# Kernel tuning notes

Hardware: AMD Instinct MI355X
Metric: run time of the kernel (lower is better)

The kernel has to match this reference:

```python
import jax, jax.numpy as jnp
import numpy as np

B, T, C = 2, 1024, 1024
E, F, K = 8, 2048, 2


def setup_inputs() -> dict:
    key = jax.random.key(0)
    ks = jax.random.split(key, 5)
    s = 1.0 / np.sqrt(C)
    return {
        "x": jax.random.normal(ks[0], (B, T, C), jnp.float32),
        "Wr": jax.random.normal(ks[1], (E, C), jnp.float32) * s,   # router weight [E, d_model]
        "w1": jax.random.normal(ks[2], (E, C, F), jnp.float32) * s, # gate proj per expert
        "w3": jax.random.normal(ks[3], (E, C, F), jnp.float32) * s, # up proj per expert
        "w2": jax.random.normal(ks[4], (E, F, C), jnp.float32) * (1.0 / np.sqrt(F)),  # down proj
    }


def reference(x, Wr, w1, w3, w2):
    Bq, Tq, Cq = x.shape
    flat = x.reshape(-1, Cq)                          # [N, C]
    N = flat.shape[0]
    probs = jax.nn.softmax(flat @ Wr.T, axis=-1)      # [N, E]
    topw, topi = jax.lax.top_k(probs, K)              # [N, K]
    topw = topw / jnp.sum(topw, axis=-1, keepdims=True)
    # dense gate matrix: zero for unselected experts (same math as masked loop)
    gates = jnp.zeros((N, E), flat.dtype).at[jnp.arange(N)[:, None], topi].set(topw)
    # evaluate all experts, weight by gates (gate=0 kills unrouted experts)
    h1 = jnp.einsum('nd,edf->nef', flat, w1)          # [N, E, F]
    h3 = jnp.einsum('nd,edf->nef', flat, w3)
    h = jax.nn.silu(h1) * h3
    y = jnp.einsum('nef,efd->ned', h, w2)             # [N, E, C]
    out = jnp.einsum('ned,ne->nd', y, gates)          # [N, C]
    return out.reshape(Bq, Tq, Cq)
```

## Files before the change

### kernel.cpp

```cpp
#include <hip/hip_runtime.h>
#include <math.h>

typedef _Float16 f16;
typedef _Float16 f16x2 __attribute__((ext_vector_type(2)));
typedef _Float16 f16x4 __attribute__((ext_vector_type(4)));
typedef _Float16 f16x8 __attribute__((ext_vector_type(8)));
typedef __fp16 h16x2 __attribute__((ext_vector_type(2)));
typedef float f32x4 __attribute__((ext_vector_type(4)));

#define N_TOK 2048
#define C_DIM 1024
#define E_NUM 8
#define F_DIM 2048
#define MAXTILES 40

#define WS_COUNTS    0
#define WS_OFFSETS   64
#define WS_TILESTART 128
#define WS_CURSOR    192
#define WS_TOPI      256
#define WS_TOPW      (WS_TOPI + 16384)
#define WS_ROWS      (WS_TOPW + 16384)
#define WS_SLOT      (WS_ROWS + 16384)
#define WS_X16       (1u << 20)
#define WS_H         (6u << 20)
#define WS_Y0        (23u << 20)
#define WS_Y1        (32u << 20)

__device__ __forceinline__ void glds16(const void* g, void* l) {
  __builtin_amdgcn_global_load_lds((const __attribute__((address_space(1))) void*)g,
                                   (__attribute__((address_space(3))) void*)l, 16, 0, 0);
}

__device__ __forceinline__ f16x2 pkrtz(float a, float b) {
  union { h16x2 h; f16x2 f; } u;
  u.h = __builtin_amdgcn_cvt_pkrtz(a, b);
  return u.f;
}

__global__ void cvtx_kernel(const float* __restrict__ x, f16* __restrict__ x16) {
  int i = (blockIdx.x * 256 + threadIdx.x) * 8;
  f32x4 a = *(const f32x4*)(x + i);
  f32x4 b = *(const f32x4*)(x + i + 4);
  union { f16x8 v; f16x2 h[4]; } u;
  u.h[0] = pkrtz(a[0], a[1]);
  u.h[1] = pkrtz(a[2], a[3]);
  u.h[2] = pkrtz(b[0], b[1]);
  u.h[3] = pkrtz(b[2], b[3]);
  *(f16x8*)(x16 + i) = u.v;
}

__global__ void router_kernel(const float* __restrict__ x, const float* __restrict__ Wr,
                              int* counts, int* topi, float* topw) {
  int tok = blockIdx.x * 4 + (threadIdx.x >> 6);
  int lane = threadIdx.x & 63;
  const float* xr = x + (size_t)tok * C_DIM;
  float xv[16];
#pragma unroll
  for (int i = 0; i < 16; ++i) xv[i] = xr[i * 64 + lane];
  float logit[E_NUM];
#pragma unroll
  for (int e = 0; e < E_NUM; ++e) {
    const float* wr = Wr + (size_t)e * C_DIM;
    float acc = 0.f;
#pragma unroll
    for (int i = 0; i < 16; ++i) acc += xv[i] * wr[i * 64 + lane];
#pragma unroll
    for (int s = 1; s < 64; s <<= 1) acc += __shfl_xor(acc, s, 64);
    logit[e] = acc;
  }
  if (lane == 0) {
    float m = logit[0];
#pragma unroll
    for (int e = 1; e < E_NUM; ++e) m = fmaxf(m, logit[e]);
    float p[E_NUM];
#pragma unroll
    for (int e = 0; e < E_NUM; ++e) p[e] = expf(logit[e] - m);
    float p0 = -1.f, p1 = -1.f;
    int i0 = 0, i1 = 0;
#pragma unroll
    for (int e = 0; e < E_NUM; ++e) {
      float v = p[e];
      if (v > p0) { p1 = p0; i1 = i0; p0 = v; i0 = e; }
      else if (v > p1) { p1 = v; i1 = e; }
    }
    float inv = 1.f / (p0 + p1);
    topi[2 * tok] = i0; topi[2 * tok + 1] = i1;
    topw[2 * tok] = p0 * inv; topw[2 * tok + 1] = p1 * inv;
    atomicAdd(&counts[i0], 1);
    atomicAdd(&counts[i1], 1);
  }
}

__global__ void scan_kernel(const int* counts, int* offsets, int* tilestart, int* cursor) {
  if (threadIdx.x == 0) {
    int o = 0, t = 0;
    for (int e = 0; e < E_NUM; ++e) {
      offsets[e] = o; tilestart[e] = t; cursor[e] = o;
      o += counts[e];
      t += (counts[e] + 127) >> 7;
    }
    offsets[E_NUM] = o; tilestart[E_NUM] = t;
  }
}

__global__ void scatter_kernel(const int* __restrict__ topi, int* cursor,
                               int* rows_perm, int* slot_of) {
  int n = blockIdx.x * blockDim.x + threadIdx.x;
  if (n >= N_TOK) return;
#pragma unroll
  for (int k = 0; k < 2; ++k) {
    int e = topi[2 * n + k];
    int pos = atomicAdd(&cursor[e], 1);
    rows_perm[pos] = n;
    slot_of[2 * n + k] = pos;
  }
}

__launch_bounds__(256, 2)
__global__ void upproj_kernel(const f16* __restrict__ x16,
                              const float* __restrict__ w1,
                              const float* __restrict__ w3,
                              const int* __restrict__ counts,
                              const int* __restrict__ offsets,
                              const int* __restrict__ tilestart,
                              const int* __restrict__ rows_perm,
                              f16* __restrict__ h_buf) {
  __shared__ f16 A_lds[128 * 32];
  __shared__ f16 B1_lds[128 * 32];
  __shared__ f16 B3_lds[128 * 32];

  int rt = blockIdx.y;
  int e = -1;
#pragma unroll
  for (int i = 0; i < E_NUM; ++i)
    if (rt >= tilestart[i] && rt < tilestart[i + 1]) e = i;
  if (e < 0) return;
  int row0 = (rt - tilestart[e]) * 128;
  int cnt = counts[e];
  int off = offsets[e];
  int f0 = blockIdx.x * 128;
  int t = threadIdx.x, wid = t >> 6, lane = t & 63;

  const f16* asrc[2];
#pragma unroll
  for (int p = 0; p < 2; ++p) {
    int chunk = p * 256 + t, row = chunk >> 2, cc = chunk & 3;
    int lr = row0 + row; if (lr > cnt - 1) lr = cnt - 1;
    int g = rows_perm[off + lr];
    asrc[p] = x16 + (size_t)g * C_DIM + 8 * (cc ^ ((row >> 1) & 3));
  }
  f16* adst0 = A_lds + wid * 512;
  f16* adst1 = A_lds + (4 + wid) * 512;

  int bcol = t & 127;
  int bg = t >> 7;
  int bxor = (bcol >> 1) & 3;
  const size_t eb = (size_t)e * C_DIM * F_DIM;
  const float* w1p = w1 + eb + (size_t)(bg * 16) * F_DIM + f0 + bcol;
  const float* w3p = w3 + eb + (size_t)(bg * 16) * F_DIM + f0 + bcol;

  f32x4 acc1[4][4] = {};
  f32x4 acc3[4][4] = {};
  int wr = (wid >> 1) * 64, wc = (wid & 1) * 64;
  int fr = lane & 15, fq = lane >> 4;

  for (int k0 = 0; k0 < C_DIM; k0 += 32) {
    __syncthreads();
    glds16(asrc[0] + k0, adst0);
    glds16(asrc[1] + k0, adst1);
    {
      float v[16];
#pragma unroll
      for (int j = 0; j < 16; ++j) v[j] = w1p[(size_t)(k0 + j) * F_DIM];
#pragma unroll
      for (int q = 0; q < 4; ++q) {
        union { f16x4 v4; f16x2 h2[2]; } u;
        u.h2[0] = pkrtz(v[q * 4 + 0], v[q * 4 + 1]);
        u.h2[1] = pkrtz(v[q * 4 + 2], v[q * 4 + 3]);
        int k = bg * 16 + q * 4;
        *(f16x4*)&B1_lds[bcol * 32 + ((k >> 3) ^ bxor) * 8 + (k & 7)] = u.v4;
      }
#pragma unroll
      for (int j = 0; j < 16; ++j) v[j] = w3p[(size_t)(k0 + j) * F_DIM];
#pragma unroll
      for (int q = 0; q < 4; ++q) {
        union { f16x4 v4; f16x2 h2[2]; } u;
        u.h2[0] = pkrtz(v[q * 4 + 0], v[q * 4 + 1]);
        u.h2[1] = pkrtz(v[q * 4 + 2], v[q * 4 + 3]);
        int k = bg * 16 + q * 4;
        *(f16x4*)&B3_lds[bcol * 32 + ((k >> 3) ^ bxor) * 8 + (k & 7)] = u.v4;
      }
    }
    __syncthreads();

    f16x8 a[4];
#pragma unroll
    for (int m = 0; m < 4; ++m) {
      int row = wr + m * 16 + fr;
      a[m] = *(const f16x8*)&A_lds[row * 32 + (fq ^ ((row >> 1) & 3)) * 8];
    }
    f16x8 b[4];
#pragma unroll
    for (int n = 0; n < 4; ++n) {
      int col = wc + n * 16 + fr;
      b[n] = *(const f16x8*)&B1_lds[col * 32 + (fq ^ ((col >> 1) & 3)) * 8];
    }
#pragma unroll
    for (int m = 0; m < 4; ++m)
#pragma unroll
      for (int n = 0; n < 4; ++n)
        acc1[m][n] = __builtin_amdgcn_mfma_f32_16x16x32_f16(a[m], b[n], acc1[m][n], 0, 0, 0);
#pragma unroll
    for (int n = 0; n < 4; ++n) {
      int col = wc + n * 16 + fr;
      b[n] = *(const f16x8*)&B3_lds[col * 32 + (fq ^ ((col >> 1) & 3)) * 8];
    }
#pragma unroll
    for (int m = 0; m < 4; ++m)
#pragma unroll
      for (int n = 0; n < 4; ++n)
        acc3[m][n] = __builtin_amdgcn_mfma_f32_16x16x32_f16(a[m], b[n], acc3[m][n], 0, 0, 0);
  }

#pragma unroll
  for (int m = 0; m < 4; ++m)
#pragma unroll
    for (int n = 0; n < 4; ++n)
#pragma unroll
      for (int i = 0; i < 4; ++i) {
        int lr = row0 + wr + m * 16 + fq * 4 + i;
        if (lr < cnt) {
          float v1 = acc1[m][n][i], v3 = acc3[m][n][i];
          float hval = v1 / (1.f + expf(-v1)) * v3;
          h_buf[(size_t)(off + lr) * F_DIM + f0 + wc + n * 16 + fr] = (f16)hval;
        }
      }
}

__launch_bounds__(256, 2)
__global__ void downproj_kernel(const f16* __restrict__ h_buf,
                                const float* __restrict__ w2,
                                const int* __restrict__ counts,
                                const int* __restrict__ offsets,
                                const int* __restrict__ tilestart,
                                f16* __restrict__ y0,
                                f16* __restrict__ y1) {
  __shared__ f16 A_lds[128 * 32];
  __shared__ f16 B_lds[128 * 32];

  int kh = blockIdx.z;
  f16* yb = kh ? y1 : y0;
  int rt = blockIdx.y;
  int e = -1;
#pragma unroll
  for (int i = 0; i < E_NUM; ++i)
    if (rt >= tilestart[i] && rt < tilestart[i + 1]) e = i;
  if (e < 0) return;
  int row0 = (rt - tilestart[e]) * 128;
  int cnt = counts[e];
  int off = offsets[e];
  int c0 = blockIdx.x * 128;
  int t = threadIdx.x, wid = t >> 6, lane = t & 63;

  const f16* asrc[2];
#pragma unroll
  for (int p = 0; p < 2; ++p) {
    int chunk = p * 256 + t, row = chunk >> 2, cc = chunk & 3;
    int lr = row0 + row; if (lr > cnt - 1) lr = cnt - 1;
    asrc[p] = h_buf + (size_t)(off + lr) * F_DIM + kh * 1024 + 8 * (cc ^ ((row >> 1) & 3));
  }
  f16* adst0 = A_lds + wid * 512;
  f16* adst1 = A_lds + (4 + wid) * 512;

  int bcol = t & 127;
  int bg = t >> 7;
  int bxor = (bcol >> 1) & 3;
  const float* w2p = w2 + (size_t)e * F_DIM * C_DIM
                     + (size_t)(kh * 1024 + bg * 16) * C_DIM + c0 + bcol;

  f32x4 acc[4][4] = {};
  int wr = (wid >> 1) * 64, wc = (wid & 1) * 64;
  int fr = lane & 15, fq = lane >> 4;

  for (int k0 = 0; k0 < 1024; k0 += 32) {
    __syncthreads();
    glds16(asrc[0] + k0, adst0);
    glds16(asrc[1] + k0, adst1);
    {
      float v[16];
#pragma unroll
      for (int j = 0; j < 16; ++j) v[j] = w2p[(size_t)(k0 + j) * C_DIM];
#pragma unroll
      for (int q = 0; q < 4; ++q) {
        union { f16x4 v4; f16x2 h2[2]; } u;
        u.h2[0] = pkrtz(v[q * 4 + 0], v[q * 4 + 1]);
        u.h2[1] = pkrtz(v[q * 4 + 2], v[q * 4 + 3]);
        int k = bg * 16 + q * 4;
        *(f16x4*)&B_lds[bcol * 32 + ((k >> 3) ^ bxor) * 8 + (k & 7)] = u.v4;
      }
    }
    __syncthreads();

    f16x8 a[4];
#pragma unroll
    for (int m = 0; m < 4; ++m) {
      int row = wr + m * 16 + fr;
      a[m] = *(const f16x8*)&A_lds[row * 32 + (fq ^ ((row >> 1) & 3)) * 8];
    }
    f16x8 b[4];
#pragma unroll
    for (int n = 0; n < 4; ++n) {
      int col = wc + n * 16 + fr;
      b[n] = *(const f16x8*)&B_lds[col * 32 + (fq ^ ((col >> 1) & 3)) * 8];
    }
#pragma unroll
    for (int m = 0; m < 4; ++m)
#pragma unroll
      for (int n = 0; n < 4; ++n)
        acc[m][n] = __builtin_amdgcn_mfma_f32_16x16x32_f16(a[m], b[n], acc[m][n], 0, 0, 0);
  }

#pragma unroll
  for (int m = 0; m < 4; ++m)
#pragma unroll
    for (int n = 0; n < 4; ++n)
#pragma unroll
      for (int i = 0; i < 4; ++i) {
        int lr = row0 + wr + m * 16 + fq * 4 + i;
        if (lr < cnt)
          yb[(size_t)(off + lr) * C_DIM + c0 + wc + n * 16 + fr] = (f16)acc[m][n][i];
      }
}

__global__ void combine_kernel(const f16* __restrict__ y0, const f16* __restrict__ y1,
                               const int* __restrict__ slot_of,
                               const float* __restrict__ topw,
                               float* __restrict__ out) {
  int n = blockIdx.x;
  int s0 = slot_of[2 * n], s1 = slot_of[2 * n + 1];
  float g0 = topw[2 * n], g1 = topw[2 * n + 1];
  int c = threadIdx.x * 4;
  f16x4 a0 = *(const f16x4*)(y0 + (size_t)s0 * C_DIM + c);
  f16x4 a1 = *(const f16x4*)(y1 + (size_t)s0 * C_DIM + c);
  f16x4 b0 = *(const f16x4*)(y0 + (size_t)s1 * C_DIM + c);
  f16x4 b1 = *(const f16x4*)(y1 + (size_t)s1 * C_DIM + c);
  f32x4 o;
#pragma unroll
  for (int i = 0; i < 4; ++i)
    o[i] = g0 * ((float)a0[i] + (float)a1[i]) + g1 * ((float)b0[i] + (float)b1[i]);
  *(f32x4*)(out + (size_t)n * C_DIM + c) = o;
}

extern "C" void kernel_launch(void* const* d_in, const int* in_sizes, int n_in,
                              void* d_out, int out_size, void* d_ws, size_t ws_size,
                              hipStream_t stream) {
  const float* x  = (const float*)d_in[0];
  const float* Wr = (const float*)d_in[1];
  const float* w1 = (const float*)d_in[2];
  const float* w3 = (const float*)d_in[3];
  const float* w2 = (const float*)d_in[4];
  float* out = (float*)d_out;
  char* ws = (char*)d_ws;

  int* counts    = (int*)(ws + WS_COUNTS);
  int* offsets   = (int*)(ws + WS_OFFSETS);
  int* tilestart = (int*)(ws + WS_TILESTART);
  int* cursor    = (int*)(ws + WS_CURSOR);
  int* topi      = (int*)(ws + WS_TOPI);
  float* topw    = (float*)(ws + WS_TOPW);
  int* rows_perm = (int*)(ws + WS_ROWS);
  int* slot_of   = (int*)(ws + WS_SLOT);
  f16* x16       = (f16*)(ws + WS_X16);
  f16* h_buf     = (f16*)(ws + WS_H);
  f16* y0        = (f16*)(ws + WS_Y0);
  f16* y1        = (f16*)(ws + WS_Y1);

  (void)hipMemsetAsync(ws, 0, 256, stream);
  cvtx_kernel<<<N_TOK * C_DIM / 8 / 256, 256, 0, stream>>>(x, x16);
  router_kernel<<<N_TOK / 4, 256, 0, stream>>>(x, Wr, counts, topi, topw);
  scan_kernel<<<1, 64, 0, stream>>>(counts, offsets, tilestart, cursor);
  scatter_kernel<<<N_TOK / 256, 256, 0, stream>>>(topi, cursor, rows_perm, slot_of);
  upproj_kernel<<<dim3(F_DIM / 128, MAXTILES), 256, 0, stream>>>(
      x16, w1, w3, counts, offsets, tilestart, rows_perm, h_buf);
  downproj_kernel<<<dim3(C_DIM / 128, MAXTILES, 2), 256, 0, stream>>>(
      h_buf, w2, counts, offsets, tilestart, y0, y1);
  combine_kernel<<<N_TOK, 256, 0, stream>>>(y0, y1, slot_of, topw, out);
}
```

Before: 244.1 us.

## Double-buffer LDS and use 256-row tiles with 512-thread blocks in expert GEMMs

The up- and down-projection kernels now use 256-row M tiles with 8 waves per block, which halves the number of times each fp32 weight tile is read and converted per expert. The K loop gets two LDS buffers, and register prefetch of the next weight slice plus an async A-tile load into the other buffer overlap with the MFMA work on the current buffer. This removes one barrier per iteration. In exchange it uses more LDS and registers per block, and experts with fewer tokens waste more rows to padding at the larger tile size.

```diff
diff --git a/kernel.cpp b/kernel.cpp
--- a/kernel.cpp
+++ b/kernel.cpp
@@ -12,7 +12,8 @@
 #define C_DIM 1024
 #define E_NUM 8
 #define F_DIM 2048
-#define MAXTILES 40
+#define BM 256
+#define MAXT2 24
 
 #define WS_COUNTS    0
 #define WS_OFFSETS   64
@@ -98,7 +99,7 @@
     for (int e = 0; e < E_NUM; ++e) {
       offsets[e] = o; tilestart[e] = t; cursor[e] = o;
       o += counts[e];
-      t += (counts[e] + 127) >> 7;
+      t += (counts[e] + 255) >> 8;
     }
     offsets[E_NUM] = o; tilestart[E_NUM] = t;
   }
@@ -117,7 +118,7 @@
   }
 }
 
-__launch_bounds__(256, 2)
+__launch_bounds__(512, 2)
 __global__ void upproj_kernel(const f16* __restrict__ x16,
                               const float* __restrict__ w1,
                               const float* __restrict__ w3,
@@ -126,9 +127,9 @@
                               const int* __restrict__ tilestart,
                               const int* __restrict__ rows_perm,
                               f16* __restrict__ h_buf) {
-  __shared__ f16 A_lds[128 * 32];
-  __shared__ f16 B1_lds[128 * 32];
-  __shared__ f16 B3_lds[128 * 32];
+  __shared__ f16 A_lds[2][BM * 32];
+  __shared__ f16 B1_lds[2][128 * 32];
+  __shared__ f16 B3_lds[2][128 * 32];
 
   int rt = blockIdx.y;
   int e = -1;
@@ -136,75 +137,73 @@
   for (int i = 0; i < E_NUM; ++i)
     if (rt >= tilestart[i] && rt < tilestart[i + 1]) e = i;
   if (e < 0) return;
-  int row0 = (rt - tilestart[e]) * 128;
-  int cnt = counts[e];
-  int off = offsets[e];
+  int row0 = (rt - tilestart[e]) * BM;
+  int cnt = counts[e], off = offsets[e];
   int f0 = blockIdx.x * 128;
   int t = threadIdx.x, wid = t >> 6, lane = t & 63;
 
   const f16* asrc[2];
 #pragma unroll
   for (int p = 0; p < 2; ++p) {
-    int chunk = p * 256 + t, row = chunk >> 2, cc = chunk & 3;
+    int c = (p * 8 + wid) * 64 + lane;
+    int row = c >> 2, cc = c & 3;
     int lr = row0 + row; if (lr > cnt - 1) lr = cnt - 1;
     int g = rows_perm[off + lr];
     asrc[p] = x16 + (size_t)g * C_DIM + 8 * (cc ^ ((row >> 1) & 3));
   }
-  f16* adst0 = A_lds + wid * 512;
-  f16* adst1 = A_lds + (4 + wid) * 512;
-
-  int bcol = t & 127;
-  int bg = t >> 7;
-  int bxor = (bcol >> 1) & 3;
+
+  int bcol = t & 127, kg = t >> 7;
+  int bso = bcol * 32 + (kg ^ ((bcol >> 1) & 3)) * 8;
   const size_t eb = (size_t)e * C_DIM * F_DIM;
-  const float* w1p = w1 + eb + (size_t)(bg * 16) * F_DIM + f0 + bcol;
-  const float* w3p = w3 + eb + (size_t)(bg * 16) * F_DIM + f0 + bcol;
+  const float* w1p = w1 + eb + (size_t)(kg * 8) * F_DIM + f0 + bcol;
+  const float* w3p = w3 + eb + (size_t)(kg * 8) * F_DIM + f0 + bcol;
 
   f32x4 acc1[4][4] = {};
   f32x4 acc3[4][4] = {};
   int wr = (wid >> 1) * 64, wc = (wid & 1) * 64;
   int fr = lane & 15, fq = lane >> 4;
 
-  for (int k0 = 0; k0 < C_DIM; k0 += 32) {
+  float r1[8], r3[8];
+#pragma unroll
+  for (int j = 0; j < 8; ++j) {
+    r1[j] = w1p[(size_t)j * F_DIM];
+    r3[j] = w3p[(size_t)j * F_DIM];
+  }
+  glds16(asrc[0], &A_lds[0][wid * 512]);
+  glds16(asrc[1], &A_lds[0][(8 + wid) * 512]);
+
+#pragma unroll 2
+  for (int tt = 0; tt < 32; ++tt) {
+    int cur = tt & 1;
+    {
+      union { f16x8 v; f16x2 h[4]; } u;
+      u.h[0] = pkrtz(r1[0], r1[1]); u.h[1] = pkrtz(r1[2], r1[3]);
+      u.h[2] = pkrtz(r1[4], r1[5]); u.h[3] = pkrtz(r1[6], r1[7]);
+      *(f16x8*)&B1_lds[cur][bso] = u.v;
+      u.h[0] = pkrtz(r3[0], r3[1]); u.h[1] = pkrtz(r3[2], r3[3]);
+      u.h[2] = pkrtz(r3[4], r3[5]); u.h[3] = pkrtz(r3[6], r3[7]);
+      *(f16x8*)&B3_lds[cur][bso] = u.v;
+    }
     __syncthreads();
-    glds16(asrc[0] + k0, adst0);
-    glds16(asrc[1] + k0, adst1);
-    {
-      float v[16];
-#pragma unroll
-      for (int j = 0; j < 16; ++j) v[j] = w1p[(size_t)(k0 + j) * F_DIM];
-#pragma unroll
-      for (int q = 0; q < 4; ++q) {
-        union { f16x4 v4; f16x2 h2[2]; } u;
-        u.h2[0] = pkrtz(v[q * 4 + 0], v[q * 4 + 1]);
-        u.h2[1] = pkrtz(v[q * 4 + 2], v[q * 4 + 3]);
-        int k = bg * 16 + q * 4;
-        *(f16x4*)&B1_lds[bcol * 32 + ((k >> 3) ^ bxor) * 8 + (k & 7)] = u.v4;
-      }
-#pragma unroll
-      for (int j = 0; j < 16; ++j) v[j] = w3p[(size_t)(k0 + j) * F_DIM];
-#pragma unroll
-      for (int q = 0; q < 4; ++q) {
-        union { f16x4 v4; f16x2 h2[2]; } u;
-        u.h2[0] = pkrtz(v[q * 4 + 0], v[q * 4 + 1]);
-        u.h2[1] = pkrtz(v[q * 4 + 2], v[q * 4 + 3]);
-        int k = bg * 16 + q * 4;
-        *(f16x4*)&B3_lds[bcol * 32 + ((k >> 3) ^ bxor) * 8 + (k & 7)] = u.v4;
-      }
-    }
-    __syncthreads();
-
+    int knext = ((tt + 1) & 31) * 32;
+    glds16(asrc[0] + knext, &A_lds[cur ^ 1][wid * 512]);
+    glds16(asrc[1] + knext, &A_lds[cur ^ 1][(8 + wid) * 512]);
+#pragma unroll
+    for (int j = 0; j < 8; ++j) {
+      r1[j] = w1p[(size_t)(knext + j) * F_DIM];
+      r3[j] = w3p[(size_t)(knext + j) * F_DIM];
+    }
     f16x8 a[4];
 #pragma unroll
     for (int m = 0; m < 4; ++m) {
       int row = wr + m * 16 + fr;
-      a[m] = *(const f16x8*)&A_lds[row * 32 + (fq ^ ((row >> 1) & 3)) * 8];
+      a[m] = *(const f16x8*)&A_lds[cur][row * 32 + (fq ^ ((row >> 1) & 3)) * 8];
     }
     f16x8 b[4];
 #pragma unroll
     for (int n = 0; n < 4; ++n) {
       int col = wc + n * 16 + fr;
-      b[n] = *(const f16x8*)&B1_lds[col * 32 + (fq ^ ((col >> 1) & 3)) * 8];
+      b[n] = *(const f16x8*)&B1_lds[cur][col * 32 + (fq ^ ((col >> 1) & 3)) * 8];
     }
 #pragma unroll
     for (int m = 0; m < 4; ++m)
@@ -214,7 +213,7 @@
 #pragma unroll
     for (int n = 0; n < 4; ++n) {
       int col = wc + n * 16 + fr;
-      b[n] = *(const f16x8*)&B3_lds[col * 32 + (fq ^ ((col >> 1) & 3)) * 8];
+      b[n] = *(const f16x8*)&B3_lds[cur][col * 32 + (fq ^ ((col >> 1) & 3)) * 8];
     }
 #pragma unroll
     for (int m = 0; m < 4; ++m)
@@ -238,7 +237,7 @@
       }
 }
 
-__launch_bounds__(256, 2)
+__launch_bounds__(512, 2)
 __global__ void downproj_kernel(const f16* __restrict__ h_buf,
                                 const float* __restrict__ w2,
                                 const int* __restrict__ counts,
@@ -246,8 +245,8 @@
                                 const int* __restrict__ tilestart,
                                 f16* __restrict__ y0,
                                 f16* __restrict__ y1) {
-  __shared__ f16 A_lds[128 * 32];
-  __shared__ f16 B_lds[128 * 32];
+  __shared__ f16 A_lds[2][BM * 32];
+  __shared__ f16 B_lds[2][128 * 32];
 
   int kh = blockIdx.z;
   f16* yb = kh ? y1 : y0;
@@ -257,62 +256,61 @@
   for (int i = 0; i < E_NUM; ++i)
     if (rt >= tilestart[i] && rt < tilestart[i + 1]) e = i;
   if (e < 0) return;
-  int row0 = (rt - tilestart[e]) * 128;
-  int cnt = counts[e];
-  int off = offsets[e];
+  int row0 = (rt - tilestart[e]) * BM;
+  int cnt = counts[e], off = offsets[e];
   int c0 = blockIdx.x * 128;
   int t = threadIdx.x, wid = t >> 6, lane = t & 63;
 
   const f16* asrc[2];
 #pragma unroll
   for (int p = 0; p < 2; ++p) {
-    int chunk = p * 256 + t, row = chunk >> 2, cc = chunk & 3;
+    int c = (p * 8 + wid) * 64 + lane;
+    int row = c >> 2, cc = c & 3;
     int lr = row0 + row; if (lr > cnt - 1) lr = cnt - 1;
     asrc[p] = h_buf + (size_t)(off + lr) * F_DIM + kh * 1024 + 8 * (cc ^ ((row >> 1) & 3));
   }
-  f16* adst0 = A_lds + wid * 512;
-  f16* adst1 = A_lds + (4 + wid) * 512;
-
-  int bcol = t & 127;
-  int bg = t >> 7;
-  int bxor = (bcol >> 1) & 3;
+
+  int bcol = t & 127, kg = t >> 7;
+  int bso = bcol * 32 + (kg ^ ((bcol >> 1) & 3)) * 8;
   const float* w2p = w2 + (size_t)e * F_DIM * C_DIM
-                     + (size_t)(kh * 1024 + bg * 16) * C_DIM + c0 + bcol;
+                     + (size_t)(kh * 1024 + kg * 8) * C_DIM + c0 + bcol;
 
   f32x4 acc[4][4] = {};
   int wr = (wid >> 1) * 64, wc = (wid & 1) * 64;
   int fr = lane & 15, fq = lane >> 4;
 
-  for (int k0 = 0; k0 < 1024; k0 += 32) {
+  float rb[8];
+#pragma unroll
+  for (int j = 0; j < 8; ++j) rb[j] = w2p[(size_t)j * C_DIM];
+  glds16(asrc[0], &A_lds[0][wid * 512]);
+  glds16(asrc[1], &A_lds[0][(8 + wid) * 512]);
+
+#pragma unroll 2
+  for (int tt = 0; tt < 32; ++tt) {
+    int cur = tt & 1;
+    {
+      union { f16x8 v; f16x2 h[4]; } u;
+      u.h[0] = pkrtz(rb[0], rb[1]); u.h[1] = pkrtz(rb[2], rb[3]);
+      u.h[2] = pkrtz(rb[4], rb[5]); u.h[3] = pkrtz(rb[6], rb[7]);
+      *(f16x8*)&B_lds[cur][bso] = u.v;
+    }
     __syncthreads();
-    glds16(asrc[0] + k0, adst0);
-    glds16(asrc[1] + k0, adst1);
-    {
-      float v[16];
-#pragma unroll
-      for (int j = 0; j < 16; ++j) v[j] = w2p[(size_t)(k0 + j) * C_DIM];
-#pragma unroll
-      for (int q = 0; q < 4; ++q) {
-        union { f16x4 v4; f16x2 h2[2]; } u;
-        u.h2[0] = pkrtz(v[q * 4 + 0], v[q * 4 + 1]);
-        u.h2[1] = pkrtz(v[q * 4 + 2], v[q * 4 + 3]);
-        int k = bg * 16 + q * 4;
-        *(f16x4*)&B_lds[bcol * 32 + ((k >> 3) ^ bxor) * 8 + (k & 7)] = u.v4;
-      }
-    }
-    __syncthreads();
-
+    int knext = ((tt + 1) & 31) * 32;
+    glds16(asrc[0] + knext, &A_lds[cur ^ 1][wid * 512]);
+    glds16(asrc[1] + knext, &A_lds[cur ^ 1][(8 + wid) * 512]);
+#pragma unroll
+    for (int j = 0; j < 8; ++j) rb[j] = w2p[(size_t)(knext + j) * C_DIM];
     f16x8 a[4];
 #pragma unroll
     for (int m = 0; m < 4; ++m) {
       int row = wr + m * 16 + fr;
-      a[m] = *(const f16x8*)&A_lds[row * 32 + (fq ^ ((row >> 1) & 3)) * 8];
+      a[m] = *(const f16x8*)&A_lds[cur][row * 32 + (fq ^ ((row >> 1) & 3)) * 8];
     }
     f16x8 b[4];
 #pragma unroll
     for (int n = 0; n < 4; ++n) {
       int col = wc + n * 16 + fr;
-      b[n] = *(const f16x8*)&B_lds[col * 32 + (fq ^ ((col >> 1) & 3)) * 8];
+      b[n] = *(const f16x8*)&B_lds[cur][col * 32 + (fq ^ ((col >> 1) & 3)) * 8];
     }
 #pragma unroll
     for (int m = 0; m < 4; ++m)
@@ -381,9 +379,9 @@
   router_kernel<<<N_TOK / 4, 256, 0, stream>>>(x, Wr, counts, topi, topw);
   scan_kernel<<<1, 64, 0, stream>>>(counts, offsets, tilestart, cursor);
   scatter_kernel<<<N_TOK / 256, 256, 0, stream>>>(topi, cursor, rows_perm, slot_of);
-  upproj_kernel<<<dim3(F_DIM / 128, MAXTILES), 256, 0, stream>>>(
+  upproj_kernel<<<dim3(F_DIM / 128, MAXT2), 512, 0, stream>>>(
       x16, w1, w3, counts, offsets, tilestart, rows_perm, h_buf);
-  downproj_kernel<<<dim3(C_DIM / 128, MAXTILES, 2), 256, 0, stream>>>(
+  downproj_kernel<<<dim3(C_DIM / 128, MAXT2, 2), 512, 0, stream>>>(
       h_buf, w2, counts, offsets, tilestart, y0, y1);
   combine_kernel<<<N_TOK, 256, 0, stream>>>(y0, y1, slot_of, topw, out);
 }
```

New measurement: 215.0 us. -11.9%, faster.
